# Kernel optimization log

Hardware: AMD Instinct MI355X
Metric: run time of the kernel (lower is better)

Reference implementation:

```python
import jax, jax.numpy as jnp
import numpy as np


def setup_inputs() -> dict:
    key = jax.random.key(0)
    ks = jax.random.split(key, 7)
    C, Cq = 128, 16  # channels, channels//8
    B, H, W = 8, 64, 64
    s = 0.05
    return {
        "x": jax.random.normal(ks[0], (B, C, H, W), jnp.float32),
        "wq": jax.random.normal(ks[1], (Cq, C), jnp.float32) * s,
        "bq": jnp.zeros((Cq,), jnp.float32),
        "wk": jax.random.normal(ks[2], (Cq, C), jnp.float32) * s,
        "bk": jnp.zeros((Cq,), jnp.float32),
        "wv": jax.random.normal(ks[3], (C, C), jnp.float32) * s,
        "bv": jnp.zeros((C,), jnp.float32),
    }


def reference(x, wq, bq, wk, bk, wv, bv):
    B, C, H, W = x.shape
    N = H * W
    dk = wq.shape[0]  # channels // 8
    xf = x.reshape(B, C, N)  # [B, C, N]
    # 1x1 convs == per-pixel linear maps over channels
    q = jnp.einsum('oc,bcn->bon', wq, xf) + bq[None, :, None]  # [B, dk, N]
    k = jnp.einsum('oc,bcn->bon', wk, xf) + bk[None, :, None]  # [B, dk, N]
    v = jnp.einsum('oc,bcn->bon', wv, xf) + bv[None, :, None]  # [B, C, N]
    # scores[b,i,j] = <q[:,i], k[:,j]> / sqrt(dk)
    scores = jnp.einsum('bdi,bdj->bij', q, k) / jnp.sqrt(jnp.asarray(dk, x.dtype))
    attn = jax.nn.softmax(scores, axis=-1)  # softmax over key dim j
    # out[b,c,i] = sum_j v[b,c,j] * attn[b,i,j]
    out = jnp.einsum('bcj,bij->bci', v, attn)
    return out.reshape(B, C, H, W) + x
```

## Files before the change

### kernel.cpp

```cpp
#include <hip/hip_runtime.h>
#include <hip/hip_bf16.h>

#define BATCH 8
#define CDIM  128
#define DK    16
#define NPIX  4096
#define VSTR  72

typedef __attribute__((ext_vector_type(4)))  float    f32x4;
typedef __attribute__((ext_vector_type(16))) float    f32x16;
typedef __attribute__((ext_vector_type(8)))  short    s16x8;
typedef __attribute__((ext_vector_type(4)))  unsigned u32x4;

__device__ __forceinline__ short f2bf(float f) {
    union { float fv; unsigned u; } un; un.fv = f;
    unsigned r = un.u + 0x7FFFu + ((un.u >> 16) & 1u);
    return (short)(r >> 16);
}
__device__ __forceinline__ float bf2f(short s) {
    union { unsigned u; float f; } un; un.u = ((unsigned)(unsigned short)s) << 16;
    return un.f;
}
__device__ __forceinline__ float fexp2(float x) {
#if __has_builtin(__builtin_amdgcn_exp2f)
    return __builtin_amdgcn_exp2f(x);
#else
    return exp2f(x);
#endif
}
__device__ __forceinline__ unsigned pkbf(float lo, float hi) {
    __hip_bfloat162 h = __float22bfloat162_rn(make_float2(lo, hi));
    return *reinterpret_cast<unsigned*>(&h);
}
__device__ __forceinline__ f32x16 zero16() {
    f32x16 z;
    #pragma unroll
    for (int i = 0; i < 16; ++i) z[i] = 0.f;
    return z;
}

#define C2F 0.36067376022224085f
#define WPFRAGS (10 * 4 * 64)

__global__ __launch_bounds__(256) void wprep(
    const float* __restrict__ wq, const float* __restrict__ wk,
    const float* __restrict__ wv, short* __restrict__ Wp)
{
    const int mt   = blockIdx.x;
    const int t    = threadIdx.x;
    const int kt   = t >> 6;
    const int lane = t & 63;
    const int m    = mt * 16 + (lane & 15);
    const int c0   = kt * 32 + ((lane >> 4) << 3);

    const float* src; float scl = 1.f;
    if (m < 16)      { src = wq + m * CDIM; scl = C2F; }
    else if (m < 32) { src = wk + (m - 16) * CDIM; }
    else             { src = wv + (m - 32) * CDIM; }

    s16x8 frag;
    #pragma unroll
    for (int i = 0; i < 8; ++i) frag[i] = f2bf(src[c0 + i] * scl);
    *(s16x8*)(Wp + (((size_t)(mt * 4 + kt) * 64 + lane) << 3)) = frag;
}

__global__ __launch_bounds__(256) void qkv_proj(
    const float* __restrict__ x, const short* __restrict__ Wp,
    const float* __restrict__ bq, const float* __restrict__ bk,
    const float* __restrict__ bv,
    short* __restrict__ Qt, short* __restrict__ Kt, short* __restrict__ Vb)
{
    const int tid   = threadIdx.x;
    const int bid   = blockIdx.x;
    const int b     = bid >> 6;
    const int nbase = (bid & 63) << 6;

    const int lane = tid & 63;
    const int lo   = lane & 15;
    const int hi   = lane >> 4;
    const int n    = ((tid >> 6) << 4) + lo;
    const int ng   = nbase + n;

    const float* xb = x + (((size_t)(b * CDIM)) << 12) + ng;

    s16x8 bfr[4];
    #pragma unroll
    for (int kt = 0; kt < 4; ++kt) {
        const float* xp = xb + (((size_t)(kt * 32 + hi * 8)) << 12);
        float v0 = xp[0];
        float v1 = xp[(size_t)1 << 12];
        float v2 = xp[(size_t)2 << 12];
        float v3 = xp[(size_t)3 << 12];
        float v4 = xp[(size_t)4 << 12];
        float v5 = xp[(size_t)5 << 12];
        float v6 = xp[(size_t)6 << 12];
        float v7 = xp[(size_t)7 << 12];
        union { u32x4 u; s16x8 v; } pk;
        pk.u[0] = pkbf(v0, v1); pk.u[1] = pkbf(v2, v3);
        pk.u[2] = pkbf(v4, v5); pk.u[3] = pkbf(v6, v7);
        bfr[kt] = pk.v;
    }

    f32x4 acc[10];
    #pragma unroll
    for (int mt = 0; mt < 10; ++mt) { acc[mt][0]=0.f; acc[mt][1]=0.f; acc[mt][2]=0.f; acc[mt][3]=0.f; }

    #pragma unroll
    for (int kt = 0; kt < 4; ++kt) {
        #pragma unroll
        for (int mt = 0; mt < 10; ++mt) {
            const s16x8 af = *(const s16x8*)(Wp + (((size_t)(mt * 4 + kt) * 64 + lane) << 3));
            acc[mt] = __builtin_amdgcn_mfma_f32_16x16x32_bf16(af, bfr[kt], acc[mt], 0, 0, 0);
        }
    }

    const int m4 = hi << 2;
    {
        uint2 pk;
        pk.x = pkbf(acc[0][0] + bq[m4 + 0] * C2F, acc[0][1] + bq[m4 + 1] * C2F);
        pk.y = pkbf(acc[0][2] + bq[m4 + 2] * C2F, acc[0][3] + bq[m4 + 3] * C2F);
        *(uint2*)(Qt + ((((size_t)(b << 12)) + ng) << 4) + m4) = pk;
    }
    {
        uint2 pk;
        pk.x = pkbf(acc[1][0] + bk[m4 + 0], acc[1][1] + bk[m4 + 1]);
        pk.y = pkbf(acc[1][2] + bk[m4 + 2], acc[1][3] + bk[m4 + 3]);
        *(uint2*)(Kt + ((((size_t)(b << 12)) + ng) << 4) + m4) = pk;
    }
    #pragma unroll
    for (int mt = 2; mt < 10; ++mt) {
        #pragma unroll
        for (int r = 0; r < 4; ++r) {
            const int c = (mt - 2) * 16 + m4 + r;
            Vb[(((size_t)(b * CDIM + c)) << 12) + ng] = f2bf(acc[mt][r] + bv[c]);
        }
    }
}

template<int KSPLIT, bool DIRECT>
__global__ __launch_bounds__(256, 2) void attn_part(
    const short* __restrict__ Qt, const short* __restrict__ Kt,
    const short* __restrict__ Vb, const float* __restrict__ x,
    float* __restrict__ out, short* __restrict__ Op, float* __restrict__ lsum)
{
    constexpr int NKEY = NPIX / KSPLIT;
    constexpr int NT   = NKEY / 64;
    __shared__ __align__(16) short vs[2][CDIM * VSTR];

    const int tid = threadIdx.x;
    const int bid = blockIdx.x;
    const int qb  = bid & 15;
    const int kc  = (bid >> 4) % KSPLIT;
    const int b   = bid / (16 * KSPLIT);
    const int q0A = qb * 256 + (tid >> 6) * 32;
    const int q0B = q0A + 128;
    const int l31 = tid & 31;
    const int hi2 = (tid >> 5) & 1;
    const int kq  = hi2 << 3;
    const int pi  = (l31 & ~12) | ((l31 & 4) << 1) | ((l31 & 8) >> 1);

    const s16x8 qBA = *(const s16x8*)(Qt + (((size_t)(b << 12) + q0A + l31) << 4) + kq);
    const s16x8 qBB = *(const s16x8*)(Qt + (((size_t)(b << 12) + q0B + l31) << 4) + kq);

    const int j8  = tid & 7;
    const int cb8 = tid >> 3;
    const short* vsrc = Vb + (((size_t)(b * CDIM + cb8)) << 12) + (j8 << 3);
    const int vdoff = cb8 * VSTR + (j8 << 3);
    const size_t cstr = (size_t)32 << 12;

    const int jbase0 = kc * NKEY;
    const short* ktb = Kt + ((size_t)(b << 12) << 4);

    f32x16 OA0 = zero16(), OA1 = zero16(), OA2 = zero16(), OA3 = zero16();
    f32x16 OB0 = zero16(), OB1 = zero16(), OB2 = zero16(), OB3 = zero16();
    float l_accA = 0.f, l_accB = 0.f;

    s16x8 r0, r1, r2, r3;
    #define VLOAD(jb) do {                                   \
        r0 = *(const s16x8*)(vsrc + (jb));                   \
        r1 = *(const s16x8*)(vsrc + (jb) + cstr);            \
        r2 = *(const s16x8*)(vsrc + (jb) + 2 * cstr);        \
        r3 = *(const s16x8*)(vsrc + (jb) + 3 * cstr);        \
    } while (0)
    #define VSTORE(bufi) do {                                \
        short* vd_ = &vs[bufi][vdoff];                       \
        *(s16x8*)(vd_)             = r0;                     \
        *(s16x8*)(vd_ + 32 * VSTR) = r1;                     \
        *(s16x8*)(vd_ + 64 * VSTR) = r2;                     \
        *(s16x8*)(vd_ + 96 * VSTR) = r3;                     \
    } while (0)
    #define KLOAD(jb) (*(const s16x8*)(ktb + (((size_t)((jb) + pi)) << 4) + kq))
    #define LDSV(vb_, ct, ch) (*(const s16x8*)((vb_) + ((ct) * 32 + l31) * VSTR + ((ch) << 3)))
    #define LOADVF(dst, h, vb_) do {                         \
        const int ch_ = ((h) << 1) | hi2;                    \
        dst[0] = LDSV(vb_, 0, ch_);                          \
        dst[1] = LDSV(vb_, 1, ch_);                          \
        dst[2] = LDSV(vb_, 2, ch_);                          \
        dst[3] = LDSV(vb_, 3, ch_);                          \
    } while (0)

    #define HALFP(sv, ktl, vf, Oa, Ob, Oc, Od, lac) do {                        \
        float p0 = fexp2(sv[8*(ktl)+0]), p1 = fexp2(sv[8*(ktl)+1]);            \
        float p2 = fexp2(sv[8*(ktl)+2]), p3 = fexp2(sv[8*(ktl)+3]);            \
        float p4 = fexp2(sv[8*(ktl)+4]), p5 = fexp2(sv[8*(ktl)+5]);            \
        float p6 = fexp2(sv[8*(ktl)+6]), p7 = fexp2(sv[8*(ktl)+7]);            \
        lac += ((p0+p1)+(p2+p3)) + ((p4+p5)+(p6+p7));                          \
        union { u32x4 u; s16x8 v; } pc_;                                       \
        pc_.u[0] = pkbf(p0,p1); pc_.u[1] = pkbf(p2,p3);                        \
        pc_.u[2] = pkbf(p4,p5); pc_.u[3] = pkbf(p6,p7);                        \
        Oa = __builtin_amdgcn_mfma_f32_32x32x16_bf16(vf[0], pc_.v, Oa, 0,0,0); \
        Ob = __builtin_amdgcn_mfma_f32_32x32x16_bf16(vf[1], pc_.v, Ob, 0,0,0); \
        Oc = __builtin_amdgcn_mfma_f32_32x32x16_bf16(vf[2], pc_.v, Oc, 0,0,0); \
        Od = __builtin_amdgcn_mfma_f32_32x32x16_bf16(vf[3], pc_.v, Od, 0,0,0); \
    } while (0)
    #define HALF_A(sv, ktl, vf) HALFP(sv, ktl, vf, OA0, OA1, OA2, OA3, l_accA)
    #define HALF_B(sv, ktl, vf) HALFP(sv, ktl, vf, OB0, OB1, OB2, OB3, l_accB)

    VLOAD(jbase0);
    s16x8 kA0c = KLOAD(jbase0);
    s16x8 kA1c = KLOAD(jbase0 + 32);
    VSTORE(0);
    __syncthreads();

    for (int t = 0; t < NT; ++t) {
        const int jb  = jbase0 + (t << 6);
        const int cur = t & 1;
        const short* vcur = &vs[cur][0];

        s16x8 vfA[4], vfB[4];
        LOADVF(vfA, 0, vcur);

        f32x16 s0a = __builtin_amdgcn_mfma_f32_32x32x16_bf16(kA0c, qBA, zero16(), 0, 0, 0);
        f32x16 s0b = __builtin_amdgcn_mfma_f32_32x32x16_bf16(kA0c, qBB, zero16(), 0, 0, 0);

        if (t + 1 < NT) VLOAD(jb + 64);

        LOADVF(vfB, 1, vcur);
        HALF_A(s0a, 0, vfA);
        HALF_B(s0b, 0, vfA);
        LOADVF(vfA, 2, vcur);
        HALF_A(s0a, 1, vfB);
        HALF_B(s0b, 1, vfB);

        f32x16 s1a = __builtin_amdgcn_mfma_f32_32x32x16_bf16(kA1c, qBA, zero16(), 0, 0, 0);
        f32x16 s1b = __builtin_amdgcn_mfma_f32_32x32x16_bf16(kA1c, qBB, zero16(), 0, 0, 0);
        if (t + 1 < NT) {
            kA0c = KLOAD(jb + 64);
            kA1c = KLOAD(jb + 96);
        }
        LOADVF(vfB, 3, vcur);
        HALF_A(s1a, 0, vfA);
        HALF_B(s1b, 0, vfA);
        HALF_A(s1a, 1, vfB);
        HALF_B(s1b, 1, vfB);

        if (t + 1 < NT) VSTORE(cur ^ 1);
        __syncthreads();
    }

    float l_totA = l_accA + __shfl_xor(l_accA, 32);
    float l_totB = l_accB + __shfl_xor(l_accB, 32);
    const int ncolA = q0A + l31;
    const int ncolB = q0B + l31;

    if constexpr (DIRECT) {
        const float invA = 1.f / l_totA;
        const float invB = 1.f / l_totB;
        #define EPID(Ov, ct, ncol, inv) do {                                   \
            _Pragma("unroll")                                                  \
            for (int r = 0; r < 16; ++r) {                                     \
                const int c = (ct)*32 + (r&3) + 8*(r>>2) + (hi2<<2);           \
                const size_t off = (((size_t)(b * CDIM + c)) << 12) + (ncol);  \
                out[off] = Ov[r] * (inv) + x[off];                             \
            } } while (0)
        EPID(OA0, 0, ncolA, invA); EPID(OA1, 1, ncolA, invA);
        EPID(OA2, 2, ncolA, invA); EPID(OA3, 3, ncolA, invA);
        EPID(OB0, 0, ncolB, invB); EPID(OB1, 1, ncolB, invB);
        EPID(OB2, 2, ncolB, invB); EPID(OB3, 3, ncolB, invB);
    } else {
        const int prow = (kc * 8 + b) * CDIM;
        #define EPIP(Ov, ct, ncol) do {                                        \
            _Pragma("unroll")                                                  \
            for (int r = 0; r < 16; ++r) {                                     \
                const int c = (ct)*32 + (r&3) + 8*(r>>2) + (hi2<<2);           \
                Op[(((size_t)(prow + c)) << 12) + (ncol)] = f2bf(Ov[r]);       \
            } } while (0)
        EPIP(OA0, 0, ncolA); EPIP(OA1, 1, ncolA);
        EPIP(OA2, 2, ncolA); EPIP(OA3, 3, ncolA);
        EPIP(OB0, 0, ncolB); EPIP(OB1, 1, ncolB);
        EPIP(OB2, 2, ncolB); EPIP(OB3, 3, ncolB);
        if (!hi2) {
            lsum[(((size_t)(kc * 8 + b)) << 12) + ncolA] = l_totA;
            lsum[(((size_t)(kc * 8 + b)) << 12) + ncolB] = l_totB;
        }
    }
}

template<int KSPLIT>
__global__ __launch_bounds__(256) void attn_combine(
    const short* __restrict__ Op, const float* __restrict__ lsum,
    const float* __restrict__ x, float* __restrict__ out)
{
    __shared__ float linv[256];
    const int tid = threadIdx.x;
    const int bid = blockIdx.x;
    const int b   = bid >> 7;
    const int nb  = (bid >> 3) & 15;
    const int cb  = bid & 7;
    const int nbase = nb << 8;

    {
        float s = 0.f;
        #pragma unroll
        for (int k = 0; k < KSPLIT; ++k)
            s += lsum[(((size_t)(k * 8 + b)) << 12) + nbase + tid];
        linv[tid] = 1.f / s;
    }
    __syncthreads();

    const int n8 = (tid & 31) << 3;
    #pragma unroll
    for (int pass = 0; pass < 2; ++pass) {
        const int c = (cb << 4) + (pass << 3) + (tid >> 5);
        const size_t gbase = (((size_t)(b * CDIM + c)) << 12) + nbase + n8;
        float acc[8];
        #pragma unroll
        for (int j = 0; j < 8; ++j) acc[j] = 0.f;
        #pragma unroll
        for (int k = 0; k < KSPLIT; ++k) {
            s16x8 v = *(const s16x8*)(Op + (((size_t)((k * 8 + b) * CDIM + c)) << 12) + nbase + n8);
            #pragma unroll
            for (int j = 0; j < 8; ++j) acc[j] += bf2f(v[j]);
        }
        float4 li0 = *(const float4*)&linv[n8];
        float4 li1 = *(const float4*)&linv[n8 + 4];
        float4 x0  = *(const float4*)(x + gbase);
        float4 x1  = *(const float4*)(x + gbase + 4);
        float4 o0, o1;
        o0.x = acc[0] * li0.x + x0.x;  o0.y = acc[1] * li0.y + x0.y;
        o0.z = acc[2] * li0.z + x0.z;  o0.w = acc[3] * li0.w + x0.w;
        o1.x = acc[4] * li1.x + x1.x;  o1.y = acc[5] * li1.y + x1.y;
        o1.z = acc[6] * li1.z + x1.z;  o1.w = acc[7] * li1.w + x1.w;
        *(float4*)(out + gbase)     = o0;
        *(float4*)(out + gbase + 4) = o1;
    }
}

extern "C" void kernel_launch(void* const* d_in, const int* in_sizes, int n_in,
                              void* d_out, int out_size, void* d_ws, size_t ws_size,
                              hipStream_t stream) {
    const float* x  = (const float*)d_in[0];
    const float* wq = (const float*)d_in[1];
    const float* bq = (const float*)d_in[2];
    const float* wk = (const float*)d_in[3];
    const float* bk = (const float*)d_in[4];
    const float* wv = (const float*)d_in[5];
    const float* bv = (const float*)d_in[6];
    float* out = (float*)d_out;

    short* Qt = (short*)d_ws;
    short* Kt = Qt + (size_t)BATCH * NPIX * DK;
    short* Vw = Kt + (size_t)BATCH * NPIX * DK;
    short* Wpk = Vw + (size_t)BATCH * CDIM * NPIX;
    char*  extra = (char*)(Wpk + (size_t)WPFRAGS * 8);
    const size_t used    = (size_t)(extra - (char*)d_ws);
    const size_t opBytes = (size_t)BATCH * CDIM * NPIX * sizeof(short);
    const size_t lBytes  = (size_t)BATCH * NPIX * sizeof(float);

    wprep<<<dim3(10), dim3(256), 0, stream>>>(wq, wk, wv, Wpk);
    qkv_proj<<<dim3(512), dim3(256), 0, stream>>>(x, Wpk, bq, bk, bv, Qt, Kt, Vw);

    if (used + 4 * (opBytes + lBytes) <= ws_size) {
        short* Opw = (short*)extra;
        float* ls  = (float*)(extra + 4 * opBytes);
        attn_part<4, false><<<dim3(8 * 16 * 4), dim3(256), 0, stream>>>(Qt, Kt, Vw, x, out, Opw, ls);
        attn_combine<4><<<dim3(1024), dim3(256), 0, stream>>>(Opw, ls, x, out);
    } else if (used + 2 * (opBytes + lBytes) <= ws_size) {
        short* Opw = (short*)extra;
        float* ls  = (float*)(extra + 2 * opBytes);
        attn_part<2, false><<<dim3(8 * 16 * 2), dim3(256), 0, stream>>>(Qt, Kt, Vw, x, out, Opw, ls);
        attn_combine<2><<<dim3(1024), dim3(256), 0, stream>>>(Opw, ls, x, out);
    } else {
        attn_part<1, true><<<dim3(8 * 16), dim3(256), 0, stream>>>(Qt, Kt, Vw, x, out, nullptr, nullptr);
    }
}
```

Before: 70.76 us.

## Pre-pack V into MFMA fragment layout and read it directly from global memory

The projection kernel now writes V in a fragment-packed layout (per 64-key tile, per 8-key chunk, per channel, 8 keys contiguous). The attention kernel then loads V MFMA operands straight from global memory/L2, dropping the LDS double buffer and the per-tile __syncthreads. It also raises wave priority around the MFMA bursts and reorders block indices so batch varies fastest. The cost is more redundant global/L2 traffic for V, since every wave loads its own fragments, and scattered 2-byte stores in the projection kernel. Loads are also no longer prefetched a tile ahead. Note that with b = bid & 7 and kc = bid >> 7, the DIRECT path (grid of 128) always gets kc = 0, which is correct.

```diff
diff --git a/kernel.cpp b/kernel.cpp
--- a/kernel.cpp
+++ b/kernel.cpp
@@ -5,7 +5,6 @@
 #define CDIM  128
 #define DK    16
 #define NPIX  4096
-#define VSTR  72
 
 typedef __attribute__((ext_vector_type(4)))  float    f32x4;
 typedef __attribute__((ext_vector_type(16))) float    f32x16;
@@ -68,7 +67,7 @@
     const float* __restrict__ x, const short* __restrict__ Wp,
     const float* __restrict__ bq, const float* __restrict__ bk,
     const float* __restrict__ bv,
-    short* __restrict__ Qt, short* __restrict__ Kt, short* __restrict__ Vb)
+    short* __restrict__ Qt, short* __restrict__ Kt, short* __restrict__ Vp)
 {
     const int tid   = threadIdx.x;
     const int bid   = blockIdx.x;
@@ -127,12 +126,16 @@
         pk.y = pkbf(acc[1][2] + bk[m4 + 2], acc[1][3] + bk[m4 + 3]);
         *(uint2*)(Kt + ((((size_t)(b << 12)) + ng) << 4) + m4) = pk;
     }
-    #pragma unroll
-    for (int mt = 2; mt < 10; ++mt) {
-        #pragma unroll
-        for (int r = 0; r < 4; ++r) {
-            const int c = (mt - 2) * 16 + m4 + r;
-            Vb[(((size_t)(b * CDIM + c)) << 12) + ng] = f2bf(acc[mt][r] + bv[c]);
+    {
+        short* vpb = Vp + ((((size_t)(b * 64 + (ng >> 6)) * 8 + ((ng >> 3) & 7)) * 128) << 3)
+                        + (ng & 7);
+        #pragma unroll
+        for (int mt = 2; mt < 10; ++mt) {
+            #pragma unroll
+            for (int r = 0; r < 4; ++r) {
+                const int c = (mt - 2) * 16 + m4 + r;
+                vpb[c << 3] = f2bf(acc[mt][r] + bv[c]);
+            }
         }
     }
 }
@@ -140,18 +143,17 @@
 template<int KSPLIT, bool DIRECT>
 __global__ __launch_bounds__(256, 2) void attn_part(
     const short* __restrict__ Qt, const short* __restrict__ Kt,
-    const short* __restrict__ Vb, const float* __restrict__ x,
+    const short* __restrict__ Vp, const float* __restrict__ x,
     float* __restrict__ out, short* __restrict__ Op, float* __restrict__ lsum)
 {
     constexpr int NKEY = NPIX / KSPLIT;
     constexpr int NT   = NKEY / 64;
-    __shared__ __align__(16) short vs[2][CDIM * VSTR];
 
     const int tid = threadIdx.x;
     const int bid = blockIdx.x;
-    const int qb  = bid & 15;
-    const int kc  = (bid >> 4) % KSPLIT;
-    const int b   = bid / (16 * KSPLIT);
+    const int b   = bid & 7;
+    const int qb  = (bid >> 3) & 15;
+    const int kc  = bid >> 7;
     const int q0A = qb * 256 + (tid >> 6) * 32;
     const int q0B = q0A + 128;
     const int l31 = tid & 31;
@@ -162,41 +164,22 @@
     const s16x8 qBA = *(const s16x8*)(Qt + (((size_t)(b << 12) + q0A + l31) << 4) + kq);
     const s16x8 qBB = *(const s16x8*)(Qt + (((size_t)(b << 12) + q0B + l31) << 4) + kq);
 
-    const int j8  = tid & 7;
-    const int cb8 = tid >> 3;
-    const short* vsrc = Vb + (((size_t)(b * CDIM + cb8)) << 12) + (j8 << 3);
-    const int vdoff = cb8 * VSTR + (j8 << 3);
-    const size_t cstr = (size_t)32 << 12;
-
     const int jbase0 = kc * NKEY;
     const short* ktb = Kt + ((size_t)(b << 12) << 4);
+    const short* vX = Vp + (((size_t)(b * 64) * 8 * 128) << 3) + (l31 << 3);
 
     f32x16 OA0 = zero16(), OA1 = zero16(), OA2 = zero16(), OA3 = zero16();
     f32x16 OB0 = zero16(), OB1 = zero16(), OB2 = zero16(), OB3 = zero16();
     float l_accA = 0.f, l_accB = 0.f;
 
-    s16x8 r0, r1, r2, r3;
-    #define VLOAD(jb) do {                                   \
-        r0 = *(const s16x8*)(vsrc + (jb));                   \
-        r1 = *(const s16x8*)(vsrc + (jb) + cstr);            \
-        r2 = *(const s16x8*)(vsrc + (jb) + 2 * cstr);        \
-        r3 = *(const s16x8*)(vsrc + (jb) + 3 * cstr);        \
-    } while (0)
-    #define VSTORE(bufi) do {                                \
-        short* vd_ = &vs[bufi][vdoff];                       \
-        *(s16x8*)(vd_)             = r0;                     \
-        *(s16x8*)(vd_ + 32 * VSTR) = r1;                     \
-        *(s16x8*)(vd_ + 64 * VSTR) = r2;                     \
-        *(s16x8*)(vd_ + 96 * VSTR) = r3;                     \
-    } while (0)
     #define KLOAD(jb) (*(const s16x8*)(ktb + (((size_t)((jb) + pi)) << 4) + kq))
-    #define LDSV(vb_, ct, ch) (*(const s16x8*)((vb_) + ((ct) * 32 + l31) * VSTR + ((ch) << 3)))
-    #define LOADVF(dst, h, vb_) do {                         \
+    #define VFRAG(tg, ch, ct) (*(const s16x8*)(vX + ((size_t)(((tg) * 8 + (ch)) << 10) + ((ct) << 8))))
+    #define LOADVF(dst, tg, h) do {                          \
         const int ch_ = ((h) << 1) | hi2;                    \
-        dst[0] = LDSV(vb_, 0, ch_);                          \
-        dst[1] = LDSV(vb_, 1, ch_);                          \
-        dst[2] = LDSV(vb_, 2, ch_);                          \
-        dst[3] = LDSV(vb_, 3, ch_);                          \
+        dst[0] = VFRAG(tg, ch_, 0);                          \
+        dst[1] = VFRAG(tg, ch_, 1);                          \
+        dst[2] = VFRAG(tg, ch_, 2);                          \
+        dst[3] = VFRAG(tg, ch_, 3);                          \
     } while (0)
 
     #define HALFP(sv, ktl, vf, Oa, Ob, Oc, Od, lac) do {                        \
@@ -208,39 +191,35 @@
         union { u32x4 u; s16x8 v; } pc_;                                       \
         pc_.u[0] = pkbf(p0,p1); pc_.u[1] = pkbf(p2,p3);                        \
         pc_.u[2] = pkbf(p4,p5); pc_.u[3] = pkbf(p6,p7);                        \
+        __builtin_amdgcn_s_setprio(1);                                          \
         Oa = __builtin_amdgcn_mfma_f32_32x32x16_bf16(vf[0], pc_.v, Oa, 0,0,0); \
         Ob = __builtin_amdgcn_mfma_f32_32x32x16_bf16(vf[1], pc_.v, Ob, 0,0,0); \
         Oc = __builtin_amdgcn_mfma_f32_32x32x16_bf16(vf[2], pc_.v, Oc, 0,0,0); \
         Od = __builtin_amdgcn_mfma_f32_32x32x16_bf16(vf[3], pc_.v, Od, 0,0,0); \
+        __builtin_amdgcn_s_setprio(0);                                          \
     } while (0)
     #define HALF_A(sv, ktl, vf) HALFP(sv, ktl, vf, OA0, OA1, OA2, OA3, l_accA)
     #define HALF_B(sv, ktl, vf) HALFP(sv, ktl, vf, OB0, OB1, OB2, OB3, l_accB)
 
-    VLOAD(jbase0);
     s16x8 kA0c = KLOAD(jbase0);
     s16x8 kA1c = KLOAD(jbase0 + 32);
-    VSTORE(0);
-    __syncthreads();
 
     for (int t = 0; t < NT; ++t) {
-        const int jb  = jbase0 + (t << 6);
-        const int cur = t & 1;
-        const short* vcur = &vs[cur][0];
-
-        s16x8 vfA[4], vfB[4];
-        LOADVF(vfA, 0, vcur);
+        const int jb = jbase0 + (t << 6);
+        const int tg = jb >> 6;
+
+        s16x8 vf0[4], vf1[4];
+        LOADVF(vf0, tg, 0);
 
         f32x16 s0a = __builtin_amdgcn_mfma_f32_32x32x16_bf16(kA0c, qBA, zero16(), 0, 0, 0);
         f32x16 s0b = __builtin_amdgcn_mfma_f32_32x32x16_bf16(kA0c, qBB, zero16(), 0, 0, 0);
 
-        if (t + 1 < NT) VLOAD(jb + 64);
-
-        LOADVF(vfB, 1, vcur);
-        HALF_A(s0a, 0, vfA);
-        HALF_B(s0b, 0, vfA);
-        LOADVF(vfA, 2, vcur);
-        HALF_A(s0a, 1, vfB);
-        HALF_B(s0b, 1, vfB);
+        LOADVF(vf1, tg, 1);
+        HALF_A(s0a, 0, vf0);
+        HALF_B(s0b, 0, vf0);
+        LOADVF(vf0, tg, 2);
+        HALF_A(s0a, 1, vf1);
+        HALF_B(s0b, 1, vf1);
 
         f32x16 s1a = __builtin_amdgcn_mfma_f32_32x32x16_bf16(kA1c, qBA, zero16(), 0, 0, 0);
         f32x16 s1b = __builtin_amdgcn_mfma_f32_32x32x16_bf16(kA1c, qBB, zero16(), 0, 0, 0);
@@ -248,14 +227,11 @@
             kA0c = KLOAD(jb + 64);
             kA1c = KLOAD(jb + 96);
         }
-        LOADVF(vfB, 3, vcur);
-        HALF_A(s1a, 0, vfA);
-        HALF_B(s1b, 0, vfA);
-        HALF_A(s1a, 1, vfB);
-        HALF_B(s1b, 1, vfB);
-
-        if (t + 1 < NT) VSTORE(cur ^ 1);
-        __syncthreads();
+        LOADVF(vf1, tg, 3);
+        HALF_A(s1a, 0, vf0);
+        HALF_B(s1b, 0, vf0);
+        HALF_A(s1a, 1, vf1);
+        HALF_B(s1b, 1, vf1);
     }
 
     float l_totA = l_accA + __shfl_xor(l_accA, 32);
@@ -360,27 +336,27 @@
 
     short* Qt = (short*)d_ws;
     short* Kt = Qt + (size_t)BATCH * NPIX * DK;
-    short* Vw = Kt + (size_t)BATCH * NPIX * DK;
-    short* Wpk = Vw + (size_t)BATCH * CDIM * NPIX;
+    short* Vp = Kt + (size_t)BATCH * NPIX * DK;
+    short* Wpk = Vp + (size_t)BATCH * CDIM * NPIX;
     char*  extra = (char*)(Wpk + (size_t)WPFRAGS * 8);
     const size_t used    = (size_t)(extra - (char*)d_ws);
     const size_t opBytes = (size_t)BATCH * CDIM * NPIX * sizeof(short);
     const size_t lBytes  = (size_t)BATCH * NPIX * sizeof(float);
 
     wprep<<<dim3(10), dim3(256), 0, stream>>>(wq, wk, wv, Wpk);
-    qkv_proj<<<dim3(512), dim3(256), 0, stream>>>(x, Wpk, bq, bk, bv, Qt, Kt, Vw);
+    qkv_proj<<<dim3(512), dim3(256), 0, stream>>>(x, Wpk, bq, bk, bv, Qt, Kt, Vp);
 
     if (used + 4 * (opBytes + lBytes) <= ws_size) {
         short* Opw = (short*)extra;
         float* ls  = (float*)(extra + 4 * opBytes);
-        attn_part<4, false><<<dim3(8 * 16 * 4), dim3(256), 0, stream>>>(Qt, Kt, Vw, x, out, Opw, ls);
+        attn_part<4, false><<<dim3(8 * 16 * 4), dim3(256), 0, stream>>>(Qt, Kt, Vp, x, out, Opw, ls);
         attn_combine<4><<<dim3(1024), dim3(256), 0, stream>>>(Opw, ls, x, out);
     } else if (used + 2 * (opBytes + lBytes) <= ws_size) {
         short* Opw = (short*)extra;
         float* ls  = (float*)(extra + 2 * opBytes);
-        attn_part<2, false><<<dim3(8 * 16 * 2), dim3(256), 0, stream>>>(Qt, Kt, Vw, x, out, Opw, ls);
+        attn_part<2, false><<<dim3(8 * 16 * 2), dim3(256), 0, stream>>>(Qt, Kt, Vp, x, out, Opw, ls);
         attn_combine<2><<<dim3(1024), dim3(256), 0, stream>>>(Opw, ls, x, out);
     } else {
-        attn_part<1, true><<<dim3(8 * 16), dim3(256), 0, stream>>>(Qt, Kt, Vw, x, out, nullptr, nullptr);
-    }
-}
+        attn_part<1, true><<<dim3(8 * 16), dim3(256), 0, stream>>>(Qt, Kt, Vp, x, out, nullptr, nullptr);
+    }
+}
```

Result: slower. 73.59 us (median of 2 runs) (+4.0%).
